# Kernel tuning notes

Measured on AMD Instinct MI355X. Metric: run time of the kernel, lower is better.

The kernel has to match this reference:

```python
import jax, jax.numpy as jnp
import numpy as np

BOUNDARY_THRESHOLD = 0.5
TARGET_N = 6.0          # target_avg_token_length
RATIO_LOSS_WEIGHT = 0.03
LR_DIFF = 0.75          # learning_rate_difference
EPS = 1e-8              # torch cosine_similarity eps


def setup_inputs() -> dict:
    key = jax.random.key(0)
    k1, k2, k3 = jax.random.split(key, 3)
    B, L, D, DK = 8, 4096, 1024, 1024
    tokens = jax.random.normal(k1, (B, L, D), dtype=jnp.float32)
    W_qk = jax.random.normal(k2, (D, 2 * DK), dtype=jnp.float32) / np.sqrt(D).astype(np.float32)
    start_key = jax.random.normal(k3, (DK,), dtype=jnp.float32) * 0.01
    return {"tokens": tokens, "W_qk": W_qk, "start_key": start_key}


def _forward(tokens, W_qk, start_key):
    B, L, D = tokens.shape
    qk = tokens @ W_qk                                   # [B, L, 2*Dk]
    queries, keys = jnp.split(qk, 2, axis=-1)
    # keys shifted right by one, with learned start key prepended
    keys_for_sim = jnp.concatenate(
        [jnp.broadcast_to(start_key, (B, 1, keys.shape[-1])), keys[:, :-1]], axis=1)
    qn = jnp.maximum(jnp.linalg.norm(queries, axis=-1), EPS)
    kn = jnp.maximum(jnp.linalg.norm(keys_for_sim, axis=-1), EPS)
    cosine_sim = jnp.sum(queries * keys_for_sim, axis=-1) / (qn * kn)   # [B, L]
    probs = (1.0 - cosine_sim) * 0.5

    boundary_mask = probs > BOUNDARY_THRESHOLD
    boundary_mask = boundary_mask.at[:, 0].set(True)     # first step: first token is boundary
    num_chunks = jnp.sum(boundary_mask, axis=-1)         # [B]

    ar = jnp.arange(L)
    valid = ar[None, :] < num_chunks[:, None]            # [B, L] mask of valid (non-pad) chunks

    # chunk_lens via sorted boundary positions with end sentinel (pads -> length 0)
    bm_end = jnp.concatenate([boundary_mask, jnp.ones((B, 1), dtype=bool)], axis=1)  # [B, L+1]
    pos = jnp.sort(jnp.where(bm_end, jnp.arange(L + 1)[None, :], L + 1), axis=-1)
    chunk_lens = jnp.where(valid, pos[:, 1:] - pos[:, :-1], 0)          # [B, L]

    # compact boundary tokens / probs to the front (pad_sequence equivalent, padded to L)
    bpos = jnp.sort(jnp.where(boundary_mask, ar[None, :], L), axis=-1)  # [B, L]
    safe = jnp.minimum(bpos, L - 1)
    boundary_tokens = jnp.where(valid[..., None],
                                jnp.take_along_axis(tokens, safe[..., None], axis=1), 0.0)
    boundary_probs = jnp.where(valid, jnp.take_along_axis(probs, safe, axis=1), 0.0)
    downsampled = boundary_tokens * boundary_probs[..., None]

    # aux ratio loss (straight-through soft fraction)
    F_hard = boundary_mask.astype(probs.dtype)
    F_soft = jax.nn.sigmoid(probs - BOUNDARY_THRESHOLD)
    F = F_soft + jax.lax.stop_gradient(F_hard - F_soft)
    G = jnp.mean(probs, axis=-1)
    Fm = jnp.mean(F, axis=-1)
    N = TARGET_N
    aux_ratio_loss = N / (N - 1.0) * ((N - 1.0) * Fm * G + (1.0 - Fm) * (1.0 - G))
    weighted_aux_loss = jnp.mean(aux_ratio_loss) * RATIO_LOSS_WEIGHT

    # frac_gradient with frac = 1 / learning_rate_difference (identity fwd, scaled grad)
    frac = 1.0 / LR_DIFF
    ds_scaled = downsampled * frac
    downsampled = ds_scaled + jax.lax.stop_gradient(downsampled - ds_scaled)

    return downsampled, chunk_lens, weighted_aux_loss


def reference(tokens, W_qk, start_key):
    return _forward(tokens, W_qk, start_key)
```

## Files before the change

kernel.cpp:

```cpp
#include <hip/hip_runtime.h>
#include <hip/hip_bf16.h>
#include <hip/hip_fp16.h>


#define B_ 8
#define L_ 4096
#define D_ 1024
#define M_TOT (B_ * L_)
#define BM 128
#define DS_ELEMS ((size_t)M_TOT * D_)
#define SUS_CAP 2048

typedef _Float16 f16x8 __attribute__((ext_vector_type(8)));
typedef _Float16 f16x4 __attribute__((ext_vector_type(4)));
typedef __bf16  bf16x8 __attribute__((ext_vector_type(8)));
typedef __bf16  bf16x4 __attribute__((ext_vector_type(4)));
typedef float   f32x4  __attribute__((ext_vector_type(4)));

typedef __attribute__((address_space(1))) void gv_t;
typedef __attribute__((address_space(3))) void lv_t;

__device__ __forceinline__ void gl_lds16(const void* g, void* l) {
    __builtin_amdgcn_global_load_lds((gv_t*)g, (lv_t*)l, 16, 0, 0);
}

__global__ __launch_bounds__(256)
void prep(const float* __restrict__ tokens, const float* __restrict__ W,
          _Float16* __restrict__ t_h, _Float16* __restrict__ wT_h,
          __bf16* __restrict__ wT_hi, __bf16* __restrict__ wT_lo,
          float* __restrict__ zbase, float* __restrict__ aux_out)
{
    const int bid = blockIdx.x, tid = threadIdx.x;
    if (bid < 8192) {
        const size_t base = (size_t)bid * 4096 + tid * 4;
        #pragma unroll
        for (int r = 0; r < 4; ++r) {
            size_t idx = base + (size_t)r * 1024;
            float4 v = *(const float4*)&tokens[idx];
            f16x4 h;
            h[0] = (_Float16)v.x; h[1] = (_Float16)v.y;
            h[2] = (_Float16)v.z; h[3] = (_Float16)v.w;
            *(f16x4*)&t_h[idx] = h;
        }
    } else if (bid < 10240) {
        __shared__ float lw[32 * 33];
        const int local = bid - 8192;
        const int k0 = (local & 31) * 32;
        const int n0 = (local >> 5) * 32;
        {
            const int lk = tid >> 3, ln4 = (tid & 7) * 4;
            float4 v = *(const float4*)&W[(size_t)(k0 + lk) * 2048 + n0 + ln4];
            lw[(ln4 + 0) * 33 + lk] = v.x;
            lw[(ln4 + 1) * 33 + lk] = v.y;
            lw[(ln4 + 2) * 33 + lk] = v.z;
            lw[(ln4 + 3) * 33 + lk] = v.w;
        }
        __syncthreads();
        {
            const int ln = tid >> 3, lk4 = (tid & 7) * 4;
            f16x4 h; bf16x4 bh, bl;
            #pragma unroll
            for (int j = 0; j < 4; ++j) {
                float v = lw[ln * 33 + lk4 + j];
                h[j] = (_Float16)v;
                __bf16 b = (__bf16)v;
                bh[j] = b;
                bl[j] = (__bf16)(v - (float)b);
            }
            size_t o = (size_t)(n0 + ln) * 1024 + k0 + lk4;
            *(f16x4*)&wT_h[o]   = h;
            *(bf16x4*)&wT_hi[o] = bh;
            *(bf16x4*)&wT_lo[o] = bl;
        }
    } else {
        const int zb = bid - 10240;
        const int i = zb * 1024 + tid * 4;
        if (i < 98308)
            *(float4*)&zbase[i] = make_float4(0.f, 0.f, 0.f, 0.f);
        if (zb == 0 && tid == 0) *aux_out = 0.f;
    }
}

__global__ __launch_bounds__(256, 4)
void gemm_cos_f16(const _Float16* __restrict__ t_h, const _Float16* __restrict__ wT_h,
                  float* __restrict__ dotw, float* __restrict__ qn2w,
                  float* __restrict__ ksn2w,
                  float* __restrict__ qrow, float* __restrict__ krow)
{
    __shared__ float smem[10240];
    float* Ck = smem;

    const int bx = blockIdx.x;
    const int tile_n = (bx >> 3) & 15;
    const int tile_m = ((bx >> 7) & 31) + ((bx & 7) << 5);
    const int m0 = tile_m * BM;
    const int n0 = tile_n * 64;
    const int tid  = threadIdx.x;
    const int w    = tid >> 6;
    const int lane = tid & 63;
    const int quad = lane >> 4;
    const int lc   = lane & 15;

    const int wm  = (w & 1) * 64;
    const int wq0 = (w >> 1) * 32;

    const int ia0 = w * 2, ia1 = w * 2 + 1;
    const int st_ch = ((lane & 3) ^ ((lane >> 3) & 3)) * 8;
    const size_t a_g0 = (size_t)(m0 + ia0 * 16 + (lane >> 2)) * 1024 + st_ch;
    const size_t a_g1 = a_g0 + (size_t)16 * 1024;
    const int br0 = ia0 * 16 + (lane >> 2);
    const int br1 = br0 + 16;
    const int gr0 = (br0 < 64) ? (n0 + br0) : (960 + n0 + br0);
    const int gr1 = (br1 < 64) ? (n0 + br1) : (960 + n0 + br1);
    const size_t b_g0 = (size_t)gr0 * 1024 + st_ch;
    const size_t b_g1 = (size_t)gr1 * 1024 + st_ch;

    char* const sb = (char*)smem;
    const int fr_ch = (quad ^ ((lc >> 1) & 3)) * 8;

    f32x4 accq[4][2] = {};
    f32x4 acck[4][2] = {};

    gl_lds16(t_h  + a_g0,      sb + ia0 * 1024);
    gl_lds16(t_h  + a_g1,      sb + ia1 * 1024);
    gl_lds16(wT_h + b_g0,      sb + 24576 + ia0 * 1024);
    gl_lds16(wT_h + b_g1,      sb + 24576 + ia1 * 1024);
    gl_lds16(t_h  + a_g0 + 32, sb + 8192 + ia0 * 1024);
    gl_lds16(t_h  + a_g1 + 32, sb + 8192 + ia1 * 1024);

    int acur = 0;
    int apre = 2;
    for (int kk = 0; kk < 32; ++kk) {
        if (kk < 31) {
            asm volatile("s_waitcnt vmcnt(2)" ::: "memory");
        } else {
            asm volatile("s_waitcnt vmcnt(0)" ::: "memory");
        }
        __builtin_amdgcn_s_barrier();
        if (kk < 31) {
            const size_t kb = (size_t)(kk + 1) * 32;
            char* nb = sb + 24576 + ((kk + 1) & 1) * 8192;
            gl_lds16(wT_h + b_g0 + kb, nb + ia0 * 1024);
            gl_lds16(wT_h + b_g1 + kb, nb + ia1 * 1024);
        }
        if (kk < 30) {
            const size_t kb = (size_t)(kk + 2) * 32;
            char* nb = sb + apre * 8192;
            gl_lds16(t_h + a_g0 + kb, nb + ia0 * 1024);
            gl_lds16(t_h + a_g1 + kb, nb + ia1 * 1024);
        }
        const _Float16* As = (const _Float16*)(sb + acur * 8192);
        const _Float16* Bs = (const _Float16*)(sb + 24576 + (kk & 1) * 8192);

        f16x8 af[4], bq[2], bk[2];
        #pragma unroll
        for (int mi = 0; mi < 4; ++mi)
            af[mi] = *(const f16x8*)(As + (wm + mi * 16 + lc) * 32 + fr_ch);
        #pragma unroll
        for (int ni = 0; ni < 2; ++ni) {
            bq[ni] = *(const f16x8*)(Bs + (wq0 + ni * 16 + lc) * 32 + fr_ch);
            bk[ni] = *(const f16x8*)(Bs + (64 + wq0 + ni * 16 + lc) * 32 + fr_ch);
        }
        #pragma unroll
        for (int mi = 0; mi < 4; ++mi) {
            #pragma unroll
            for (int ni = 0; ni < 2; ++ni) {
                accq[mi][ni] = __builtin_amdgcn_mfma_f32_16x16x32_f16(
                    af[mi], bq[ni], accq[mi][ni], 0, 0, 0);
                acck[mi][ni] = __builtin_amdgcn_mfma_f32_16x16x32_f16(
                    af[mi], bk[ni], acck[mi][ni], 0, 0, 0);
            }
        }
        acur = (acur == 2) ? 0 : acur + 1;
        apre = (apre == 2) ? 0 : apre + 1;
    }
    __syncthreads();

    #pragma unroll
    for (int mi = 0; mi < 4; ++mi) {
        #pragma unroll
        for (int reg = 0; reg < 4; ++reg) {
            const int row = wm + mi * 16 + quad * 4 + reg;
            float s = accq[mi][0][reg] * accq[mi][0][reg]
                    + accq[mi][1][reg] * accq[mi][1][reg];
            s += __shfl_xor(s, 1); s += __shfl_xor(s, 2);
            s += __shfl_xor(s, 4); s += __shfl_xor(s, 8);
            if (lc == 0) atomicAdd(&qn2w[m0 + row], s);

            float s2 = acck[mi][0][reg] * acck[mi][0][reg]
                     + acck[mi][1][reg] * acck[mi][1][reg];
            s2 += __shfl_xor(s2, 1); s2 += __shfl_xor(s2, 2);
            s2 += __shfl_xor(s2, 4); s2 += __shfl_xor(s2, 8);
            if (lc == 0 && row < 127) atomicAdd(&ksn2w[m0 + row + 1], s2);
        }
    }

    #pragma unroll
    for (int mi = 0; mi < 4; ++mi)
        #pragma unroll
        for (int ni = 0; ni < 2; ++ni)
            #pragma unroll
            for (int reg = 0; reg < 4; ++reg)
                Ck[(wm + mi * 16 + quad * 4 + reg) * 66 + wq0 + ni * 16 + lc] =
                    acck[mi][ni][reg];
    __syncthreads();

    #pragma unroll
    for (int mi = 0; mi < 4; ++mi) {
        #pragma unroll
        for (int reg = 0; reg < 4; ++reg) {
            const int row = wm + mi * 16 + quad * 4 + reg;
            float d = 0.f;
            if (row >= 1)
                d = accq[mi][0][reg] * Ck[(row - 1) * 66 + wq0 + lc]
                  + accq[mi][1][reg] * Ck[(row - 1) * 66 + wq0 + 16 + lc];
            d += __shfl_xor(d, 1); d += __shfl_xor(d, 2);
            d += __shfl_xor(d, 4); d += __shfl_xor(d, 8);
            if (lc == 0 && row >= 1) atomicAdd(&dotw[m0 + row], d);
        }
    }

    if (wm == 0 && quad == 0) {
        #pragma unroll
        for (int ni = 0; ni < 2; ++ni)
            qrow[(size_t)tile_m * D_ + n0 + wq0 + ni * 16 + lc] = accq[0][ni][0];
    }
    if (wm == 64 && quad == 3) {
        #pragma unroll
        for (int ni = 0; ni < 2; ++ni)
            krow[(size_t)tile_m * D_ + n0 + wq0 + ni * 16 + lc] = acck[3][ni][3];
    }
}

__global__ __launch_bounds__(256)
void probs_fused(const float* __restrict__ qrow, const float* __restrict__ krow,
                 const float* __restrict__ start_key,
                 const float* __restrict__ dotw, const float* __restrict__ qn2w,
                 const float* __restrict__ ksn2w, float* __restrict__ probsw,
                 int* __restrict__ scount, int* __restrict__ slist)
{
    const int tile = blockIdx.x;
    const int tid = threadIdx.x;
    __shared__ float sd[4], sk[4];

    {
        const float* q  = qrow + (size_t)tile * D_;
        const float* ks = ((tile & 31) == 0) ? start_key
                                             : (krow + (size_t)(tile - 1) * D_);
        float4 qv = *(const float4*)&q[tid * 4];
        float4 kv = *(const float4*)&ks[tid * 4];
        float d  = qv.x * kv.x + qv.y * kv.y + qv.z * kv.z + qv.w * kv.w;
        float k2 = kv.x * kv.x + kv.y * kv.y + kv.z * kv.z + kv.w * kv.w;
        #pragma unroll
        for (int off = 32; off; off >>= 1) {
            d  += __shfl_down(d, off, 64);
            k2 += __shfl_down(k2, off, 64);
        }
        const int lane = tid & 63, wid = tid >> 6;
        if (lane == 0) { sd[wid] = d; sk[wid] = k2; }
    }
    __syncthreads();

    if (tid < BM) {
        const int m = tile * BM + tid;
        float dd = dotw[m], kk = ksn2w[m];
        if (tid == 0) {
            dd = sd[0] + sd[1] + sd[2] + sd[3];
            kk = sk[0] + sk[1] + sk[2] + sk[3];
        }
        float qn = fmaxf(sqrtf(qn2w[m]), 1e-8f);
        float kn = fmaxf(sqrtf(kk), 1e-8f);
        float c = dd / (qn * kn);
        probsw[m] = 0.5f * (1.f - c);
        if (fabsf(c) < 1e-3f) {
            int i = atomicAdd(scount, 1);
            if (i < SUS_CAP) slist[i] = m;
        }
    }
}

__global__ __launch_bounds__(256)
void gather_split(const float* __restrict__ tokens, const int* __restrict__ scount,
                  const int* __restrict__ slist,
                  __bf16* __restrict__ As_hi, __bf16* __restrict__ As_lo)
{
    int n = *scount; if (n > SUS_CAP) n = SUS_CAP;
    const int n_up = (n + 127) & ~127;
    const int slot = blockIdx.x;
    const int sl = slot & 2047;
    if (sl >= n_up) return;
    const int tid = threadIdx.x;

    int src = -1;
    if (sl < n) {
        int t = slist[sl];
        if (slot < 2048) src = t;
        else src = ((t & 4095) == 0) ? t : (t - 1);
    }
    bf16x4 h = {}, l = {};
    if (src >= 0) {
        float4 v = *(const float4*)&tokens[(size_t)src * 1024 + tid * 4];
        float vs[4] = {v.x, v.y, v.z, v.w};
        #pragma unroll
        for (int j = 0; j < 4; ++j) {
            __bf16 b = (__bf16)vs[j];
            h[j] = b;
            l[j] = (__bf16)(vs[j] - (float)b);
        }
    }
    size_t o = (size_t)slot * 1024 + tid * 4;
    *(bf16x4*)&As_hi[o] = h;
    *(bf16x4*)&As_lo[o] = l;
}

__global__ __launch_bounds__(256, 2)
void gemm2(const __bf16* __restrict__ As_hi, const __bf16* __restrict__ As_lo,
           const __bf16* __restrict__ wT_hi, const __bf16* __restrict__ wT_lo,
           const int* __restrict__ scount, float* __restrict__ C2)
{
    int n = *scount; if (n > SUS_CAP) n = SUS_CAP;
    const int tm = blockIdx.y;
    const int local_base = (tm < 16) ? tm * 128 : (tm - 16) * 128;
    if (local_base >= n) return;
    const int m0 = (tm < 16) ? tm * 128 : 2048 + (tm - 16) * 128;

    __shared__ float smem[12288];

    const int tile_n = blockIdx.x;
    const int n0 = tile_n * 128;
    const int colbase = ((tm < 16) ? 0 : 1024) + n0;
    const int tid  = threadIdx.x;
    const int w    = tid >> 6;
    const int lane = tid & 63;
    const int quad = lane >> 4;
    const int lc   = lane & 15;
    const int wm  = (w & 1) * 64;
    const int wq0 = (w >> 1) * 32;

    const int ia0 = w * 2, ia1 = w * 2 + 1;
    const int st_ch = ((lane & 3) ^ ((lane >> 3) & 3)) * 8;
    const size_t a_g0 = (size_t)(m0 + ia0 * 16 + (lane >> 2)) * 1024 + st_ch;
    const size_t a_g1 = a_g0 + (size_t)16 * 1024;
    const int br0 = ia0 * 16 + (lane >> 2);
    const int br1 = br0 + 16;
    const size_t b_g0 = (size_t)(colbase + br0) * 1024 + st_ch;
    const size_t b_g1 = (size_t)(colbase + br1) * 1024 + st_ch;

    char* const sb = (char*)smem;
    const int fr_ch = (quad ^ ((lc >> 1) & 3)) * 8;

    f32x4 accq[4][2] = {};
    f32x4 acck[4][2] = {};

    gl_lds16(As_hi + a_g0,      sb + ia0 * 1024);
    gl_lds16(As_hi + a_g1,      sb + ia1 * 1024);
    gl_lds16(wT_hi + b_g0,      sb + 8192 + ia0 * 1024);
    gl_lds16(wT_hi + b_g1,      sb + 8192 + ia1 * 1024);
    gl_lds16(As_hi + a_g0 + 32, sb + 16384 + ia0 * 1024);
    gl_lds16(As_hi + a_g1 + 32, sb + 16384 + ia1 * 1024);
    gl_lds16(wT_hi + b_g0 + 32, sb + 16384 + 8192 + ia0 * 1024);
    gl_lds16(wT_hi + b_g1 + 32, sb + 16384 + 8192 + ia1 * 1024);

    int cur = 0;
    for (int kk = 0; kk < 96; ++kk) {
        if (kk < 95) {
            asm volatile("s_waitcnt vmcnt(4)" ::: "memory");
        } else {
            asm volatile("s_waitcnt vmcnt(0)" ::: "memory");
        }
        __builtin_amdgcn_s_barrier();
        if (kk < 94) {
            const int k2 = kk + 2;
            const int slab2 = k2 >> 5;
            const size_t kb2 = (size_t)(k2 & 31) * 32;
            const __bf16* Ap2 = (slab2 < 2) ? As_hi : As_lo;
            const __bf16* Bp2 = (slab2 == 1) ? wT_lo : wT_hi;
            int nxt = cur + 2; if (nxt >= 3) nxt -= 3;
            char* nb = sb + nxt * 16384;
            gl_lds16(Ap2 + a_g0 + kb2, nb + ia0 * 1024);
            gl_lds16(Ap2 + a_g1 + kb2, nb + ia1 * 1024);
            gl_lds16(Bp2 + b_g0 + kb2, nb + 8192 + ia0 * 1024);
            gl_lds16(Bp2 + b_g1 + kb2, nb + 8192 + ia1 * 1024);
        }
        const __bf16* As = (const __bf16*)(sb + cur * 16384);
        const __bf16* Bs = As + 4096;

        bf16x8 af[4], bq[2], bk[2];
        #pragma unroll
        for (int mi = 0; mi < 4; ++mi)
            af[mi] = *(const bf16x8*)(As + (wm + mi * 16 + lc) * 32 + fr_ch);
        #pragma unroll
        for (int ni = 0; ni < 2; ++ni) {
            bq[ni] = *(const bf16x8*)(Bs + (wq0 + ni * 16 + lc) * 32 + fr_ch);
            bk[ni] = *(const bf16x8*)(Bs + (64 + wq0 + ni * 16 + lc) * 32 + fr_ch);
        }
        #pragma unroll
        for (int mi = 0; mi < 4; ++mi) {
            #pragma unroll
            for (int ni = 0; ni < 2; ++ni) {
                accq[mi][ni] = __builtin_amdgcn_mfma_f32_16x16x32_bf16(
                    af[mi], bq[ni], accq[mi][ni], 0, 0, 0);
                acck[mi][ni] = __builtin_amdgcn_mfma_f32_16x16x32_bf16(
                    af[mi], bk[ni], acck[mi][ni], 0, 0, 0);
            }
        }
        cur = (cur == 2) ? 0 : cur + 1;
    }

    #pragma unroll
    for (int mi = 0; mi < 4; ++mi) {
        #pragma unroll
        for (int reg = 0; reg < 4; ++reg) {
            const int row = m0 + wm + mi * 16 + quad * 4 + reg;
            #pragma unroll
            for (int ni = 0; ni < 2; ++ni) {
                C2[(size_t)row * 2048 + colbase + wq0 + ni * 16 + lc] = accq[mi][ni][reg];
                C2[(size_t)row * 2048 + colbase + 64 + wq0 + ni * 16 + lc] = acck[mi][ni][reg];
            }
        }
    }
}

__global__ __launch_bounds__(256)
void dot_fix(const float* __restrict__ C2, const float* __restrict__ start_key,
             const int* __restrict__ scount, const int* __restrict__ slist,
             float* __restrict__ probsw, int* __restrict__ scount2,
             int* __restrict__ slist2, float* __restrict__ fix3acc)
{
    int n = *scount; if (n > SUS_CAP) n = SUS_CAP;
    const int s = blockIdx.x;
    if (s >= n) return;
    const int tid = threadIdx.x;
    const int t = slist[s];
    const bool st = (t & 4095) == 0;
    const float* q = C2 + (size_t)s * 2048;
    const float* k = st ? start_key : (C2 + (size_t)(2048 + s) * 2048 + 1024);

    float4 qv = *(const float4*)&q[tid * 4];
    float4 kv = *(const float4*)&k[tid * 4];
    float d  = qv.x * kv.x + qv.y * kv.y + qv.z * kv.z + qv.w * kv.w;
    float q2 = qv.x * qv.x + qv.y * qv.y + qv.z * qv.z + qv.w * qv.w;
    float k2 = kv.x * kv.x + kv.y * kv.y + kv.z * kv.z + kv.w * kv.w;
    #pragma unroll
    for (int off = 32; off; off >>= 1) {
        d  += __shfl_down(d, off, 64);
        q2 += __shfl_down(q2, off, 64);
        k2 += __shfl_down(k2, off, 64);
    }
    __shared__ float sd[4], sq[4], sk[4];
    const int lane = tid & 63, wid = tid >> 6;
    if (lane == 0) { sd[wid] = d; sq[wid] = q2; sk[wid] = k2; }
    __syncthreads();
    if (tid == 0) {
        float D  = sd[0] + sd[1] + sd[2] + sd[3];
        float Q2 = sq[0] + sq[1] + sq[2] + sq[3];
        float K2 = sk[0] + sk[1] + sk[2] + sk[3];
        float c = D / (fmaxf(sqrtf(Q2), 1e-8f) * fmaxf(sqrtf(K2), 1e-8f));
        if (fabsf(c) < 1e-4f) {
            int i = atomicAdd(scount2, 1);
            if (i < SUS_CAP) {
                slist2[i] = t;
                float* fa = fix3acc + 3 * i;
                fa[0] = 0.f; fa[1] = 0.f; fa[2] = 0.f;
            }
        } else {
            probsw[t] = 0.5f * (1.f - c);
        }
    }
}

__global__ __launch_bounds__(256)
void fixup3a(const float* __restrict__ tokens, const float* __restrict__ W,
             const float* __restrict__ start_key, const int* __restrict__ scount2,
             const int* __restrict__ slist2, float* __restrict__ fix3acc)
{
    __shared__ float ta[1024], tb[1024], kvs[128];
    const int tid = threadIdx.x;
    const int lane = tid & 63;
    const int c = blockIdx.x & 7;
    int n = *scount2; if (n > SUS_CAP) n = SUS_CAP;

    for (int i = blockIdx.x >> 3; i < n; i += 128) {
        const int t = slist2[i];
        const bool st = (t & 4095) == 0;
        *(float4*)&ta[tid * 4] = *(const float4*)&tokens[(size_t)t * 1024 + tid * 4];
        if (!st)
            *(float4*)&tb[tid * 4] = *(const float4*)&tokens[(size_t)(t - 1) * 1024 + tid * 4];
        __syncthreads();

        float qd = 0.f, q2p = 0.f, k2p = 0.f, dotp = 0.f;
        if (tid < 128) {
            const float* Wp = W + c * 128 + tid;
            float a0 = 0.f, a1 = 0.f, a2 = 0.f, a3 = 0.f;
            for (int k = 0; k < 1024; k += 4) {
                a0 = fmaf(ta[k + 0], Wp[(size_t)(k + 0) * 2048], a0);
                a1 = fmaf(ta[k + 1], Wp[(size_t)(k + 1) * 2048], a1);
                a2 = fmaf(ta[k + 2], Wp[(size_t)(k + 2) * 2048], a2);
                a3 = fmaf(ta[k + 3], Wp[(size_t)(k + 3) * 2048], a3);
            }
            qd = (a0 + a1) + (a2 + a3);
            q2p = qd * qd;
        } else {
            const int j = tid - 128;
            float kd;
            if (st) {
                kd = start_key[c * 128 + j];
            } else {
                const float* Wp = W + 1024 + c * 128 + j;
                float a0 = 0.f, a1 = 0.f, a2 = 0.f, a3 = 0.f;
                for (int k = 0; k < 1024; k += 4) {
                    a0 = fmaf(tb[k + 0], Wp[(size_t)(k + 0) * 2048], a0);
                    a1 = fmaf(tb[k + 1], Wp[(size_t)(k + 1) * 2048], a1);
                    a2 = fmaf(tb[k + 2], Wp[(size_t)(k + 2) * 2048], a2);
                    a3 = fmaf(tb[k + 3], Wp[(size_t)(k + 3) * 2048], a3);
                }
                kd = (a0 + a1) + (a2 + a3);
            }
            kvs[j] = kd;
            k2p = kd * kd;
        }
        __syncthreads();
        if (tid < 128) dotp = qd * kvs[tid];

        #pragma unroll
        for (int off = 32; off; off >>= 1) {
            dotp += __shfl_down(dotp, off, 64);
            q2p  += __shfl_down(q2p,  off, 64);
            k2p  += __shfl_down(k2p,  off, 64);
        }
        if (lane == 0) {
            float* fa = fix3acc + 3 * i;
            atomicAdd(&fa[0], dotp);
            atomicAdd(&fa[1], q2p);
            atomicAdd(&fa[2], k2p);
        }
        __syncthreads();
    }
}

__global__ __launch_bounds__(256)
void fixup3b(const int* __restrict__ scount2, const int* __restrict__ slist2,
             const float* __restrict__ fix3acc, float* __restrict__ probsw)
{
    int n = *scount2; if (n > SUS_CAP) n = SUS_CAP;
    for (int i = threadIdx.x + blockIdx.x * 256; i < n; i += 256 * gridDim.x) {
        const int t = slist2[i];
        const float* fa = fix3acc + 3 * i;
        float D = fa[0], Q2 = fa[1], K2 = fa[2];
        float qn = fmaxf(sqrtf(Q2), 1e-8f), kn = fmaxf(sqrtf(K2), 1e-8f);
        probsw[t] = 0.5f * (1.f - D / (qn * kn));
    }
}

__global__ __launch_bounds__(1024)
void chunk_scan_p(const float* __restrict__ probsw, int* __restrict__ bposw,
                  int* __restrict__ ncw, float* __restrict__ aux_out,
                  float* __restrict__ out_lens)
{
    const int b = blockIdx.x, tid = threadIdx.x;
    const int lane = tid & 63, wid = tid >> 6;
    __shared__ int wcnt[16];
    __shared__ float wsum[16];
    __shared__ int s_nc;
    __shared__ float s_ps;

    const int base = b * L_ + tid * 4;
    float4 pv = *(const float4*)&probsw[base];
    const float p[4] = {pv.x, pv.y, pv.z, pv.w};

    bool mk[4]; int cnt = 0; float psum = 0.f;
    #pragma unroll
    for (int j = 0; j < 4; ++j) {
        mk[j] = (p[j] > 0.5f) || ((tid * 4 + j) == 0);
        cnt += mk[j] ? 1 : 0;
        psum += p[j];
    }
    int inc = cnt;
    #pragma unroll
    for (int off = 1; off < 64; off <<= 1) {
        int nn = __shfl_up(inc, off, 64);
        if (lane >= off) inc += nn;
    }
    float ps = psum;
    #pragma unroll
    for (int off = 32; off; off >>= 1) ps += __shfl_down(ps, off, 64);
    if (lane == 63) wcnt[wid] = inc;
    if (lane == 0)  wsum[wid] = ps;
    __syncthreads();
    if (tid == 0) {
        int run = 0; float tt = 0.f;
        for (int i = 0; i < 16; ++i) { int c = wcnt[i]; wcnt[i] = run; run += c; tt += wsum[i]; }
        s_nc = run; s_ps = tt;
    }
    __syncthreads();
    const int nc = s_nc;
    int idx = wcnt[wid] + (inc - cnt);
    #pragma unroll
    for (int j = 0; j < 4; ++j)
        if (mk[j]) { bposw[b * L_ + idx] = tid * 4 + j; ++idx; }
    if (tid == 0) {
        ncw[b] = nc;
        float G  = s_ps * (1.f / L_);
        float Fm = (float)nc * (1.f / L_);
        atomicAdd(aux_out, 0.0045f * (5.f * Fm * G + (1.f - Fm) * (1.f - G)));
    }
    __syncthreads();
    #pragma unroll
    for (int j = 0; j < 4; ++j) {
        int i = tid * 4 + j;
        float len = 0.f;
        if (i < nc) {
            int pi  = bposw[b * L_ + i];
            int nxt = (i + 1 < nc) ? bposw[b * L_ + i + 1] : L_;
            len = (float)(nxt - pi);
        }
        out_lens[b * L_ + i] = len;
    }
}

__global__ __launch_bounds__(256)
void gather_ds(const float* __restrict__ tokens, const float* __restrict__ probsw,
               const int* __restrict__ bposw, const int* __restrict__ ncw,
               float* __restrict__ out)
{
    const int row = blockIdx.x;
    const int b = row >> 12, i = row & 4095;
    const int nc = ncw[b];
    float4 v = make_float4(0.f, 0.f, 0.f, 0.f);
    if (i < nc) {
        const int t = bposw[b * L_ + i];
        const float pv = probsw[b * L_ + t];
        float4 tv = *(const float4*)&tokens[((size_t)(b << 12) + t) * D_ + threadIdx.x * 4];
        v = make_float4(tv.x * pv, tv.y * pv, tv.z * pv, tv.w * pv);
    }
    *(float4*)&out[(size_t)row * D_ + threadIdx.x * 4] = v;
}

extern "C" void kernel_launch(void* const* d_in, const int* in_sizes, int n_in,
                              void* d_out, int out_size, void* d_ws, size_t ws_size,
                              hipStream_t stream)
{
    const float* tokens    = (const float*)d_in[0];
    const float* W_qk      = (const float*)d_in[1];
    const float* start_key = (const float*)d_in[2];
    float* out = (float*)d_out;
    float* lens_out = out + DS_ELEMS;
    float* aux_out  = out + DS_ELEMS + M_TOT;

    float* wf = (float*)d_ws;
    float* dotw    = wf;
    float* qn2w    = wf + 32768;
    float* ksn2w   = wf + 65536;
    int*   scount  = (int*)(wf + 98304);
    int*   scount2 = (int*)(wf + 98305);
    float* probsw  = wf + 98308;
    int*   bposw   = (int*)(wf + 131076);
    int*   ncw     = (int*)(wf + 163844);
    int*   slist   = (int*)(wf + 163852);
    int*   slist2  = (int*)(wf + 165900);
    float* qrow    = wf + 167948;
    float* krow    = wf + 430092;
    _Float16* wT_h = (_Float16*)(wf + 692236);

    _Float16* t_h  = (_Float16*)out;
    __bf16* As_hi  = (__bf16*)(out + 16777216);
    __bf16* As_lo  = (__bf16*)(out + 18874368);
    float*  C2     = out + 20971520;
    __bf16* wT_hi  = (__bf16*)(out + 29360128);
    __bf16* wT_lo  = (__bf16*)(out + 30408704);
    float* fix3acc = out + 18874368;

    prep<<<10337, 256, 0, stream>>>(tokens, W_qk, t_h, wT_h, wT_hi, wT_lo,
                                    wf, aux_out);
    gemm_cos_f16<<<4096, 256, 0, stream>>>(t_h, wT_h, dotw, qn2w, ksn2w,
                                           qrow, krow);
    probs_fused<<<256, 256, 0, stream>>>(qrow, krow, start_key, dotw, qn2w,
                                         ksn2w, probsw, scount, slist);
    gather_split<<<4096, 256, 0, stream>>>(tokens, scount, slist, As_hi, As_lo);
    gemm2<<<dim3(8, 32), 256, 0, stream>>>(As_hi, As_lo, wT_hi, wT_lo,
                                           scount, C2);
    dot_fix<<<2048, 256, 0, stream>>>(C2, start_key, scount, slist, probsw,
                                      scount2, slist2, fix3acc);
    fixup3a<<<1024, 256, 0, stream>>>(tokens, W_qk, start_key, scount2, slist2,
                                      fix3acc);
    fixup3b<<<8, 256, 0, stream>>>(scount2, slist2, fix3acc, probsw);
    chunk_scan_p<<<B_, 1024, 0, stream>>>(probsw, bposw, ncw, aux_out, lens_out);
    gather_ds<<<M_TOT, 256, 0, stream>>>(tokens, probsw, bposw, ncw, out);
}
```

Before: 640.8 us.

## Widen gemm_cos N-tile to 128 q and 128 k columns per block

Each block of the fused QK GEMM now computes 128 query and 128 key columns instead of 64 each. This halves the grid to 2048 blocks and doubles the accumulators per wave. The aim is to reload each A (token) tile half as often, raise MFMA work per LDS fetch, and cut the number of atomics for norms and dot products. In exchange it uses more registers and LDS (launch bounds drop to 2 blocks per SM), which lowers occupancy and may weaken latency hiding.

```diff
diff --git a/kernel.cpp b/kernel.cpp
--- a/kernel.cpp
+++ b/kernel.cpp
@@ -81,20 +81,20 @@
     }
 }
 
-__global__ __launch_bounds__(256, 4)
+__global__ __launch_bounds__(256, 2)
 void gemm_cos_f16(const _Float16* __restrict__ t_h, const _Float16* __restrict__ wT_h,
                   float* __restrict__ dotw, float* __restrict__ qn2w,
                   float* __restrict__ ksn2w,
                   float* __restrict__ qrow, float* __restrict__ krow)
 {
-    __shared__ float smem[10240];
+    __shared__ float smem[16640];
     float* Ck = smem;
 
     const int bx = blockIdx.x;
-    const int tile_n = (bx >> 3) & 15;
-    const int tile_m = ((bx >> 7) & 31) + ((bx & 7) << 5);
+    const int tile_n = (bx >> 3) & 7;
+    const int tile_m = ((bx >> 6) & 31) + ((bx & 7) << 5);
     const int m0 = tile_m * BM;
-    const int n0 = tile_n * 64;
+    const int n0 = tile_n * 128;
     const int tid  = threadIdx.x;
     const int w    = tid >> 6;
     const int lane = tid & 63;
@@ -102,31 +102,45 @@
     const int lc   = lane & 15;
 
     const int wm  = (w & 1) * 64;
-    const int wq0 = (w >> 1) * 32;
-
+    const int wq0 = (w >> 1) * 64;
+
+    const int st_ch = ((lane & 3) ^ ((lane >> 3) & 3)) * 8;
     const int ia0 = w * 2, ia1 = w * 2 + 1;
-    const int st_ch = ((lane & 3) ^ ((lane >> 3) & 3)) * 8;
     const size_t a_g0 = (size_t)(m0 + ia0 * 16 + (lane >> 2)) * 1024 + st_ch;
     const size_t a_g1 = a_g0 + (size_t)16 * 1024;
-    const int br0 = ia0 * 16 + (lane >> 2);
-    const int br1 = br0 + 16;
-    const int gr0 = (br0 < 64) ? (n0 + br0) : (960 + n0 + br0);
-    const int gr1 = (br1 < 64) ? (n0 + br1) : (960 + n0 + br1);
-    const size_t b_g0 = (size_t)gr0 * 1024 + st_ch;
-    const size_t b_g1 = (size_t)gr1 * 1024 + st_ch;
-
-    char* const sb = (char*)smem;
+    size_t b_g[4];
+    #pragma unroll
+    for (int j = 0; j < 4; ++j) {
+        const int br = (w * 4 + j) * 16 + (lane >> 2);
+        const int gr = (br < 128) ? (n0 + br) : (896 + n0 + br);
+        b_g[j] = (size_t)gr * 1024 + st_ch;
+    }
+
+    char* const sb  = (char*)smem;
+    char* const sbB = sb + 24576;
     const int fr_ch = (quad ^ ((lc >> 1) & 3)) * 8;
 
-    f32x4 accq[4][2] = {};
-    f32x4 acck[4][2] = {};
-
-    gl_lds16(t_h  + a_g0,      sb + ia0 * 1024);
-    gl_lds16(t_h  + a_g1,      sb + ia1 * 1024);
-    gl_lds16(wT_h + b_g0,      sb + 24576 + ia0 * 1024);
-    gl_lds16(wT_h + b_g1,      sb + 24576 + ia1 * 1024);
-    gl_lds16(t_h  + a_g0 + 32, sb + 8192 + ia0 * 1024);
-    gl_lds16(t_h  + a_g1 + 32, sb + 8192 + ia1 * 1024);
+    f32x4 accq[4][4] = {};
+    f32x4 acck[4][4] = {};
+
+#define STAGE_A(KK, BASE)                                                    \
+    {                                                                        \
+        const size_t kb = (size_t)(KK) * 32;                                 \
+        gl_lds16(t_h + a_g0 + kb, (BASE) + ia0 * 1024);                      \
+        gl_lds16(t_h + a_g1 + kb, (BASE) + ia1 * 1024);                      \
+    }
+#define STAGE_B(KK, BASE)                                                    \
+    {                                                                        \
+        const size_t kb = (size_t)(KK) * 32;                                 \
+        gl_lds16(wT_h + b_g[0] + kb, (BASE) + (w * 4 + 0) * 1024);           \
+        gl_lds16(wT_h + b_g[1] + kb, (BASE) + (w * 4 + 1) * 1024);           \
+        gl_lds16(wT_h + b_g[2] + kb, (BASE) + (w * 4 + 2) * 1024);           \
+        gl_lds16(wT_h + b_g[3] + kb, (BASE) + (w * 4 + 3) * 1024);           \
+    }
+
+    STAGE_A(0, sb)
+    STAGE_B(0, sbB)
+    STAGE_A(1, sb + 8192)
 
     int acur = 0;
     int apre = 2;
@@ -137,34 +151,25 @@
             asm volatile("s_waitcnt vmcnt(0)" ::: "memory");
         }
         __builtin_amdgcn_s_barrier();
-        if (kk < 31) {
-            const size_t kb = (size_t)(kk + 1) * 32;
-            char* nb = sb + 24576 + ((kk + 1) & 1) * 8192;
-            gl_lds16(wT_h + b_g0 + kb, nb + ia0 * 1024);
-            gl_lds16(wT_h + b_g1 + kb, nb + ia1 * 1024);
-        }
-        if (kk < 30) {
-            const size_t kb = (size_t)(kk + 2) * 32;
-            char* nb = sb + apre * 8192;
-            gl_lds16(t_h + a_g0 + kb, nb + ia0 * 1024);
-            gl_lds16(t_h + a_g1 + kb, nb + ia1 * 1024);
-        }
+        if (kk < 31) STAGE_B(kk + 1, sbB + ((kk + 1) & 1) * 16384)
+        if (kk < 30) STAGE_A(kk + 2, sb + apre * 8192)
+
         const _Float16* As = (const _Float16*)(sb + acur * 8192);
-        const _Float16* Bs = (const _Float16*)(sb + 24576 + (kk & 1) * 8192);
-
-        f16x8 af[4], bq[2], bk[2];
+        const _Float16* Bs = (const _Float16*)(sbB + (kk & 1) * 16384);
+
+        f16x8 af[4], bq[4], bk[4];
         #pragma unroll
         for (int mi = 0; mi < 4; ++mi)
             af[mi] = *(const f16x8*)(As + (wm + mi * 16 + lc) * 32 + fr_ch);
         #pragma unroll
-        for (int ni = 0; ni < 2; ++ni) {
+        for (int ni = 0; ni < 4; ++ni) {
             bq[ni] = *(const f16x8*)(Bs + (wq0 + ni * 16 + lc) * 32 + fr_ch);
-            bk[ni] = *(const f16x8*)(Bs + (64 + wq0 + ni * 16 + lc) * 32 + fr_ch);
+            bk[ni] = *(const f16x8*)(Bs + (128 + wq0 + ni * 16 + lc) * 32 + fr_ch);
         }
         #pragma unroll
         for (int mi = 0; mi < 4; ++mi) {
             #pragma unroll
-            for (int ni = 0; ni < 2; ++ni) {
+            for (int ni = 0; ni < 4; ++ni) {
                 accq[mi][ni] = __builtin_amdgcn_mfma_f32_16x16x32_f16(
                     af[mi], bq[ni], accq[mi][ni], 0, 0, 0);
                 acck[mi][ni] = __builtin_amdgcn_mfma_f32_16x16x32_f16(
@@ -174,6 +179,8 @@
         acur = (acur == 2) ? 0 : acur + 1;
         apre = (apre == 2) ? 0 : apre + 1;
     }
+#undef STAGE_A
+#undef STAGE_B
     __syncthreads();
 
     #pragma unroll
@@ -181,14 +188,16 @@
         #pragma unroll
         for (int reg = 0; reg < 4; ++reg) {
             const int row = wm + mi * 16 + quad * 4 + reg;
-            float s = accq[mi][0][reg] * accq[mi][0][reg]
-                    + accq[mi][1][reg] * accq[mi][1][reg];
+            float s = 0.f, s2 = 0.f;
+            #pragma unroll
+            for (int ni = 0; ni < 4; ++ni) {
+                s  += accq[mi][ni][reg] * accq[mi][ni][reg];
+                s2 += acck[mi][ni][reg] * acck[mi][ni][reg];
+            }
             s += __shfl_xor(s, 1); s += __shfl_xor(s, 2);
             s += __shfl_xor(s, 4); s += __shfl_xor(s, 8);
             if (lc == 0) atomicAdd(&qn2w[m0 + row], s);
 
-            float s2 = acck[mi][0][reg] * acck[mi][0][reg]
-                     + acck[mi][1][reg] * acck[mi][1][reg];
             s2 += __shfl_xor(s2, 1); s2 += __shfl_xor(s2, 2);
             s2 += __shfl_xor(s2, 4); s2 += __shfl_xor(s2, 8);
             if (lc == 0 && row < 127) atomicAdd(&ksn2w[m0 + row + 1], s2);
@@ -198,10 +207,10 @@
     #pragma unroll
     for (int mi = 0; mi < 4; ++mi)
         #pragma unroll
-        for (int ni = 0; ni < 2; ++ni)
+        for (int ni = 0; ni < 4; ++ni)
             #pragma unroll
             for (int reg = 0; reg < 4; ++reg)
-                Ck[(wm + mi * 16 + quad * 4 + reg) * 66 + wq0 + ni * 16 + lc] =
+                Ck[(wm + mi * 16 + quad * 4 + reg) * 130 + wq0 + ni * 16 + lc] =
                     acck[mi][ni][reg];
     __syncthreads();
 
@@ -211,9 +220,12 @@
         for (int reg = 0; reg < 4; ++reg) {
             const int row = wm + mi * 16 + quad * 4 + reg;
             float d = 0.f;
-            if (row >= 1)
-                d = accq[mi][0][reg] * Ck[(row - 1) * 66 + wq0 + lc]
-                  + accq[mi][1][reg] * Ck[(row - 1) * 66 + wq0 + 16 + lc];
+            if (row >= 1) {
+                #pragma unroll
+                for (int ni = 0; ni < 4; ++ni)
+                    d += accq[mi][ni][reg]
+                       * Ck[(row - 1) * 130 + wq0 + ni * 16 + lc];
+            }
             d += __shfl_xor(d, 1); d += __shfl_xor(d, 2);
             d += __shfl_xor(d, 4); d += __shfl_xor(d, 8);
             if (lc == 0 && row >= 1) atomicAdd(&dotw[m0 + row], d);
@@ -222,12 +234,12 @@
 
     if (wm == 0 && quad == 0) {
         #pragma unroll
-        for (int ni = 0; ni < 2; ++ni)
+        for (int ni = 0; ni < 4; ++ni)
             qrow[(size_t)tile_m * D_ + n0 + wq0 + ni * 16 + lc] = accq[0][ni][0];
     }
     if (wm == 64 && quad == 3) {
         #pragma unroll
-        for (int ni = 0; ni < 2; ++ni)
+        for (int ni = 0; ni < 4; ++ni)
             krow[(size_t)tile_m * D_ + n0 + wq0 + ni * 16 + lc] = acck[3][ni][3];
     }
 }
@@ -672,7 +684,7 @@
 
     prep<<<10337, 256, 0, stream>>>(tokens, W_qk, t_h, wT_h, wT_hi, wT_lo,
                                     wf, aux_out);
-    gemm_cos_f16<<<4096, 256, 0, stream>>>(t_h, wT_h, dotw, qn2w, ksn2w,
+    gemm_cos_f16<<<2048, 256, 0, stream>>>(t_h, wT_h, dotw, qn2w, ksn2w,
                                            qrow, krow);
     probs_fused<<<256, 256, 0, stream>>>(qrow, krow, start_key, dotw, qn2w,
                                          ksn2w, probsw, scount, slist);
```

After: 570.9 us. 1.12x faster.
